# Performance work log

Hardware: AMD Instinct MI355X
Metric: run time of the kernel (lower is better)

The kernel has to match this reference:

```python
import jax, jax.numpy as jnp
import numpy as np

NPOINT, RADIUS, NSAMPLE, EPS = 1024, 0.2, 32, 1e-5


def furthest_point_sample(xyz, npoint):
    # xyz: [B,N,3] -> idx [B,npoint] int32. Sequential FPS starting at index 0
    # (matches pointnet2 CUDA kernel initialization).
    B, N, _ = xyz.shape
    dist0 = jnp.full((B, N), 1e10, xyz.dtype)
    far0 = jnp.zeros((B,), jnp.int32)
    idx0 = jnp.zeros((B, npoint), jnp.int32)  # idx[:,0] = 0

    def body(i, state):
        idx, dist, far = state
        centroid = jnp.take_along_axis(xyz, far[:, None, None], axis=1)  # [B,1,3]
        d = jnp.sum((xyz - centroid) ** 2, axis=-1)                       # [B,N]
        dist = jnp.minimum(dist, d)
        far = jnp.argmax(dist, axis=1).astype(jnp.int32)
        return idx.at[:, i].set(far), dist, far

    idx, _, _ = jax.lax.fori_loop(1, npoint, body, (idx0, dist0, far0))
    return idx


def ball_query(radius, nsample, xyz, new_xyz):
    # xyz [B,N,3], new_xyz [B,S,3] -> idx [B,S,nsample] int32.
    # First nsample points (in original order) within radius; slots with no
    # neighbor are filled with the first found index (standard pointnet2 semantics).
    B, N, _ = xyz.shape
    S = new_xyz.shape[1]
    d2 = (jnp.sum(new_xyz ** 2, -1)[:, :, None]
          + jnp.sum(xyz ** 2, -1)[:, None, :]
          - 2.0 * jnp.einsum('bsc,bnc->bsn', new_xyz, xyz))  # [B,S,N]
    grp = jnp.broadcast_to(jnp.arange(N, dtype=jnp.int32), (B, S, N))
    grp = jnp.where(d2 > radius * radius, N, grp)
    grp = jnp.sort(grp, axis=-1)[:, :, :nsample]
    first = grp[:, :, :1]
    return jnp.where(grp == N, first, grp)


def _gather(pts, idx):
    # pts [B,N,C], idx [B,...] -> [B,...,C]
    return jax.vmap(lambda p, i: p[i])(pts, idx)


def setup_inputs() -> dict:
    key = jax.random.key(0)
    ks = jax.random.split(key, 32)
    B, N, D = 16, 4096, 64
    mlp = [64, 64, 128]
    inp = {
        'xyz': jax.random.uniform(ks[0], (B, N, 3), jnp.float32),
        'points': jax.random.normal(ks[1], (B, N, D), jnp.float32),
    }
    cprev = 3 + D
    for i, cout in enumerate(mlp):
        kk = ks[2 + 4 * i: 6 + 4 * i]
        inp[f'W{i}'] = jax.random.normal(kk[0], (cout, cprev), jnp.float32) / np.float32(np.sqrt(cprev))
        inp[f'b{i}'] = jax.random.normal(kk[1], (cout,), jnp.float32) * 0.01
        inp[f'g{i}'] = 1.0 + 0.1 * jax.random.normal(kk[2], (cout,), jnp.float32)
        inp[f'beta{i}'] = 0.1 * jax.random.normal(kk[3], (cout,), jnp.float32)
        inp[f'm{i}'] = jnp.zeros((cout,), jnp.float32)
        inp[f'v{i}'] = jnp.ones((cout,), jnp.float32)
        cprev = cout
    return inp


def reference(xyz, points, W0, b0, g0, beta0, m0, v0,
              W1, b1, g1, beta1, m1, v1,
              W2, b2, g2, beta2, m2, v2):
    fps_idx = furthest_point_sample(xyz, NPOINT)
    new_xyz = _gather(xyz, fps_idx)                       # [B,S,3]
    idx = ball_query(RADIUS, NSAMPLE, xyz, new_xyz)       # [B,S,K]
    grouped_xyz = _gather(xyz, idx)                       # [B,S,K,3]
    grouped_norm = grouped_xyz - new_xyz[:, :, None, :]
    grouped_pts = _gather(points, idx)                    # [B,S,K,D]
    h = jnp.concatenate([grouped_norm, grouped_pts], axis=-1)  # [B,S,K,3+D]
    layers = [(W0, b0, g0, beta0, m0, v0), (W1, b1, g1, beta1, m1, v1), (W2, b2, g2, beta2, m2, v2)]
    for W, b, g, be, m, v in layers:
        h = jnp.einsum('oc,bskc->bsko', W, h) + b          # 1x1 conv
        h = (h - m) * (g * jax.lax.rsqrt(v + EPS)) + be    # eval-mode BN
        h = jax.nn.relu(h)
    new_points = jnp.max(h, axis=2)                        # max over nsample -> [B,S,Cout]
    return new_xyz, new_points
```

## Files before the change

kernel.cpp:

```cpp
#include <hip/hip_runtime.h>

#define N_PTS  4096
#define N_CENT 1024
#define K_S    32
#define EPSV   1e-5f

typedef __attribute__((ext_vector_type(8))) short short8;
typedef __attribute__((ext_vector_type(4))) float floatx4;
typedef __attribute__((ext_vector_type(2))) float float2v;

__device__ inline unsigned short bf1(float x) {
  unsigned u = __float_as_uint(x);
  u += 0x7fffu + ((u >> 16) & 1u);
  return (unsigned short)(u >> 16);
}
__device__ inline unsigned pkbf(float a, float b) {
  return (unsigned)bf1(a) | ((unsigned)bf1(b) << 16);
}

__global__ void prep_kernel(const float* __restrict__ W0, const float* __restrict__ b0,
                            const float* __restrict__ g0, const float* __restrict__ be0,
                            const float* __restrict__ m0, const float* __restrict__ v0,
                            const float* __restrict__ W1, const float* __restrict__ b1,
                            const float* __restrict__ g1, const float* __restrict__ be1,
                            const float* __restrict__ m1, const float* __restrict__ v1,
                            const float* __restrict__ W2, const float* __restrict__ b2,
                            const float* __restrict__ g2, const float* __restrict__ be2,
                            const float* __restrict__ m2, const float* __restrict__ v2,
                            unsigned char* __restrict__ wsb) {
  const int stride = gridDim.x * blockDim.x;
  const int tid = blockIdx.x * blockDim.x + threadIdx.x;
  unsigned short* WB0 = (unsigned short*)wsb;
  unsigned short* WB1 = (unsigned short*)(wsb + 12288);
  unsigned short* WB2 = (unsigned short*)(wsb + 20480);
  float* Bf0 = (float*)(wsb + 36864);
  float* Bf1 = (float*)(wsb + 37120);
  float* Bf2 = (float*)(wsb + 37376);
  for (int i = tid; i < 64 * 96; i += stride) {
    int o = i / 96, k = i - o * 96;
    float s = g0[o] * rsqrtf(v0[o] + EPSV);
    float val = 0.0f;
    if (k < 64) val = W0[o * 67 + 3 + k] * s;
    else if (k < 67) val = W0[o * 67 + (k - 64)] * s;
    WB0[i] = bf1(val);
  }
  for (int i = tid; i < 64; i += stride) {
    float s = g0[i] * rsqrtf(v0[i] + EPSV);
    Bf0[i] = (b0[i] - m0[i]) * s + be0[i];
  }
  for (int i = tid; i < 64 * 64; i += stride) {
    int o = i >> 6;
    float s = g1[o] * rsqrtf(v1[o] + EPSV);
    WB1[i] = bf1(W1[i] * s);
  }
  for (int i = tid; i < 64; i += stride) {
    float s = g1[i] * rsqrtf(v1[i] + EPSV);
    Bf1[i] = (b1[i] - m1[i]) * s + be1[i];
  }
  for (int i = tid; i < 128 * 64; i += stride) {
    int o = i >> 6;
    float s = g2[o] * rsqrtf(v2[o] + EPSV);
    WB2[i] = bf1(W2[i] * s);
  }
  for (int i = tid; i < 128; i += stride) {
    float s = g2[i] * rsqrtf(v2[i] + EPSV);
    Bf2[i] = (b2[i] - m2[i]) * s + be2[i];
  }
}

#define DPP_STEP(CTRL)                                                               \
  {                                                                                  \
    unsigned lo2 = (unsigned)__builtin_amdgcn_update_dpp(                            \
        0, (int)(unsigned)key, (CTRL), 0xf, 0xf, false);                             \
    unsigned hi2 = (unsigned)__builtin_amdgcn_update_dpp(                            \
        0, (int)(unsigned)(key >> 32), (CTRL), 0xf, 0xf, false);                     \
    unsigned long long nk = ((unsigned long long)hi2 << 32) | lo2;                   \
    if (nk > key) key = nk;                                                          \
  }

__launch_bounds__(256)
__global__ void fps_kernel(const float* __restrict__ xyz, float* __restrict__ new_xyz) {
#pragma clang fp contract(off)
  const int b = blockIdx.x;
  const int tid = threadIdx.x;
  const int lane = tid & 63, wv = tid >> 6;
  const float* X = xyz + (size_t)b * N_PTS * 3;
  __shared__ float lx[N_PTS], ly[N_PTS], lz[N_PTS];
  __shared__ float cent[N_CENT * 3];
  __shared__ unsigned long long rkey[2][4];
  float2v px[8], py[8], pz[8], dist[8];
#pragma unroll
  for (int j = 0; j < 16; ++j) {
    int p = j * 256 + tid;
    float x = X[p * 3 + 0], y = X[p * 3 + 1], z = X[p * 3 + 2];
    lx[p] = x; ly[p] = y; lz[p] = z;
    int t = j >> 1;
    if ((j & 1) == 0) { px[t].x = x; py[t].x = y; pz[t].x = z; dist[t].x = 1e10f; }
    else              { px[t].y = x; py[t].y = y; pz[t].y = z; dist[t].y = 1e10f; }
  }
  if (tid == 0) { cent[0] = X[0]; cent[1] = X[1]; cent[2] = X[2]; }
  __syncthreads();
  int far = 0;
  for (int i = 1; i < N_CENT; ++i) {
    float cx = lx[far], cy = ly[far], cz = lz[far];
    float2v cx2 = {cx, cx}, cy2 = {cy, cy}, cz2 = {cz, cz};
    float best = -1.0f;
    int bi = 0;
#pragma unroll
    for (int t = 0; t < 8; ++t) {
      float2v dx = px[t] - cx2, dy = py[t] - cy2, dz = pz[t] - cz2;
      float2v d2 = dx * dx + dy * dy + dz * dz;
      float d0 = fminf(dist[t].x, d2.x); dist[t].x = d0;
      if (d0 > best) { best = d0; bi = (2 * t) * 256 + tid; }
      float d1 = fminf(dist[t].y, d2.y); dist[t].y = d1;
      if (d1 > best) { best = d1; bi = (2 * t + 1) * 256 + tid; }
    }
    unsigned long long key =
        ((unsigned long long)__float_as_uint(best) << 32) | (unsigned)(~bi);
    DPP_STEP(0x111);
    DPP_STEP(0x112);
    DPP_STEP(0x114);
    DPP_STEP(0x118);
    DPP_STEP(0x142);
    DPP_STEP(0x143);
    const int par = i & 1;
    if (lane == 63) rkey[par][wv] = key;
    __syncthreads();
    unsigned long long k0 = rkey[par][0], k1 = rkey[par][1];
    unsigned long long k2 = rkey[par][2], k3 = rkey[par][3];
    if (k1 > k0) k0 = k1;
    if (k3 > k2) k2 = k3;
    if (k2 > k0) k0 = k2;
    far = (int)~(unsigned)k0;
    if (tid == 0) {
      cent[i * 3 + 0] = lx[far];
      cent[i * 3 + 1] = ly[far];
      cent[i * 3 + 2] = lz[far];
    }
  }
  __syncthreads();
  const size_t ob = (size_t)b * N_CENT * 3;
  for (int t = tid; t < N_CENT * 3; t += 256) new_xyz[ob + t] = cent[t];
}

__launch_bounds__(256)
__global__ void query_kernel(const float* __restrict__ xyz,
                             const float* __restrict__ new_xyz,
                             int* __restrict__ nid_g) {
#pragma clang fp contract(off)
  const int blk = blockIdx.x;
  const int b = blk >> 7;
  const int s0 = (blk & 127) << 3;
  const int tid = threadIdx.x;
  const int wv = tid >> 6, lane = tid & 63;
  const float* Xb = xyz + (size_t)b * N_PTS * 3;
  const float r2 = (float)(0.2 * 0.2);
  const int sA = s0 + wv * 2, sB = sA + 1;
  float cxA = new_xyz[((size_t)b * N_CENT + sA) * 3 + 0];
  float cyA = new_xyz[((size_t)b * N_CENT + sA) * 3 + 1];
  float czA = new_xyz[((size_t)b * N_CENT + sA) * 3 + 2];
  float cxB = new_xyz[((size_t)b * N_CENT + sB) * 3 + 0];
  float cyB = new_xyz[((size_t)b * N_CENT + sB) * 3 + 1];
  float czB = new_xyz[((size_t)b * N_CENT + sB) * 3 + 2];
  float scA = cxA * cxA + cyA * cyA + czA * czA;
  float scB = cxB * cxB + cyB * cyB + czB * czB;
  int* outA = nid_g + ((size_t)b * N_CENT + sA) * K_S;
  int* outB = nid_g + ((size_t)b * N_CENT + sB) * K_S;
  int cntA = 0, cntB = 0, firstA = 0, firstB = 0;
  for (int base = 0; base < N_PTS && (cntA < K_S || cntB < K_S); base += 64) {
    int p = base + lane;
    float x = Xb[p * 3 + 0], y = Xb[p * 3 + 1], z = Xb[p * 3 + 2];
    float sp = x * x + y * y + z * z;
    float dtA = __builtin_fmaf(czA, z, __builtin_fmaf(cyA, y, cxA * x));
    float dtB = __builtin_fmaf(czB, z, __builtin_fmaf(cyB, y, cxB * x));
    float d2A = (scA + sp) - 2.0f * dtA;
    float d2B = (scB + sp) - 2.0f * dtB;
    bool inA = !(d2A > r2);
    bool inB = !(d2B > r2);
    unsigned long long mA = __ballot(inA);
    unsigned long long mB = __ballot(inB);
    if (cntA == 0 && mA != 0ull) firstA = base + __builtin_ctzll(mA);
    if (cntB == 0 && mB != 0ull) firstB = base + __builtin_ctzll(mB);
    unsigned long long below = (1ull << lane) - 1ull;
    int posA = cntA + __popcll(mA & below);
    int posB = cntB + __popcll(mB & below);
    if (inA && posA < K_S) outA[posA] = p;
    if (inB && posB < K_S) outB[posB] = p;
    cntA += __popcll(mA);
    cntB += __popcll(mB);
  }
  if (cntA < K_S)
    for (int j = cntA + lane; j < K_S; j += 64) outA[j] = firstA;
  if (cntB < K_S)
    for (int j = cntB + lane; j < K_S; j += 64) outB[j] = firstB;
}

__launch_bounds__(256)
__global__ void mlp_kernel(const float* __restrict__ xyz,
                           const float* __restrict__ points,
                           const float* __restrict__ new_xyz,
                           const unsigned char* __restrict__ wsb,
                           const int* __restrict__ nid_g,
                           float* __restrict__ out_pts) {
  __shared__ __align__(16) unsigned short h[256 * 104];
  const int blk = blockIdx.x;
  const int b = blk >> 7;
  const int s0 = (blk & 127) << 3;
  const int tid = threadIdx.x;
  const float* Xb = xyz + (size_t)b * N_PTS * 3;

  {
    const int s = s0 + (tid >> 5);
    const int id = nid_g[((size_t)b * N_CENT + s0) * K_S + tid];
    float cx = new_xyz[((size_t)b * N_CENT + s) * 3 + 0];
    float cy = new_xyz[((size_t)b * N_CENT + s) * 3 + 1];
    float cz = new_xyz[((size_t)b * N_CENT + s) * 3 + 2];
    float gx = Xb[id * 3 + 0] - cx;
    float gy = Xb[id * 3 + 1] - cy;
    float gz = Xb[id * 3 + 2] - cz;
    unsigned short* hrow = &h[tid * 104];
    const float4* P = (const float4*)(points + ((size_t)b * N_PTS + id) * 64);
#pragma unroll
    for (int c8 = 0; c8 < 8; ++c8) {
      float4 u = P[2 * c8], v = P[2 * c8 + 1];
      uint4 w4;
      w4.x = pkbf(u.x, u.y); w4.y = pkbf(u.z, u.w);
      w4.z = pkbf(v.x, v.y); w4.w = pkbf(v.z, v.w);
      *(uint4*)(hrow + c8 * 8) = w4;
    }
    uint4 t4;
    t4.x = pkbf(gx, gy); t4.y = pkbf(gz, 0.0f); t4.z = 0u; t4.w = 0u;
    *(uint4*)(hrow + 64) = t4;
    uint4 z4; z4.x = z4.y = z4.z = z4.w = 0u;
    *(uint4*)(hrow + 72) = z4;
    *(uint4*)(hrow + 80) = z4;
    *(uint4*)(hrow + 88) = z4;
  }
  __syncthreads();

  const int lane = tid & 63, w = tid >> 6;
  const int col = lane & 15, kq = lane >> 4;
  const unsigned short* WB0 = (const unsigned short*)wsb;
  const unsigned short* WB1 = (const unsigned short*)(wsb + 12288);
  const unsigned short* WB2 = (const unsigned short*)(wsb + 20480);
  const float* Bf0 = (const float*)(wsb + 36864);
  const float* Bf1 = (const float*)(wsb + 37120);
  const float* Bf2 = (const float*)(wsb + 37376);

  {
    const int o = w * 16 + col;
    float bias = Bf0[o];
    floatx4 acc[16];
#pragma unroll
    for (int mt = 0; mt < 16; ++mt) acc[mt] = floatx4{bias, bias, bias, bias};
#pragma unroll
    for (int c = 0; c < 3; ++c) {
      short8 bf = *(const short8*)(WB0 + o * 96 + kq * 8 + 32 * c);
#pragma unroll
      for (int mt = 0; mt < 16; ++mt) {
        short8 af = *(const short8*)(&h[(mt * 16 + col) * 104 + kq * 8 + 32 * c]);
        acc[mt] = __builtin_amdgcn_mfma_f32_16x16x32_bf16(af, bf, acc[mt], 0, 0, 0);
      }
    }
    __syncthreads();
#pragma unroll
    for (int mt = 0; mt < 16; ++mt)
#pragma unroll
      for (int r = 0; r < 4; ++r)
        h[(mt * 16 + kq * 4 + r) * 104 + o] = bf1(fmaxf(acc[mt][r], 0.0f));
    __syncthreads();
  }

  {
    const int o = w * 16 + col;
    float bias = Bf1[o];
    floatx4 acc[16];
#pragma unroll
    for (int mt = 0; mt < 16; ++mt) acc[mt] = floatx4{bias, bias, bias, bias};
#pragma unroll
    for (int c = 0; c < 2; ++c) {
      short8 bf = *(const short8*)(WB1 + o * 64 + kq * 8 + 32 * c);
#pragma unroll
      for (int mt = 0; mt < 16; ++mt) {
        short8 af = *(const short8*)(&h[(mt * 16 + col) * 104 + kq * 8 + 32 * c]);
        acc[mt] = __builtin_amdgcn_mfma_f32_16x16x32_bf16(af, bf, acc[mt], 0, 0, 0);
      }
    }
    __syncthreads();
#pragma unroll
    for (int mt = 0; mt < 16; ++mt)
#pragma unroll
      for (int r = 0; r < 4; ++r)
        h[(mt * 16 + kq * 4 + r) * 104 + o] = bf1(fmaxf(acc[mt][r], 0.0f));
    __syncthreads();
  }

  {
    const int oA = w * 32 + col;
    const int oB = oA + 16;
    float biasA = Bf2[oA], biasB = Bf2[oB];
    floatx4 accA[16], accB[16];
#pragma unroll
    for (int mt = 0; mt < 16; ++mt) {
      accA[mt] = floatx4{biasA, biasA, biasA, biasA};
      accB[mt] = floatx4{biasB, biasB, biasB, biasB};
    }
#pragma unroll
    for (int c = 0; c < 2; ++c) {
      short8 bfA = *(const short8*)(WB2 + oA * 64 + kq * 8 + 32 * c);
      short8 bfB = *(const short8*)(WB2 + oB * 64 + kq * 8 + 32 * c);
#pragma unroll
      for (int mt = 0; mt < 16; ++mt) {
        short8 af = *(const short8*)(&h[(mt * 16 + col) * 104 + kq * 8 + 32 * c]);
        accA[mt] = __builtin_amdgcn_mfma_f32_16x16x32_bf16(af, bfA, accA[mt], 0, 0, 0);
        accB[mt] = __builtin_amdgcn_mfma_f32_16x16x32_bf16(af, bfB, accB[mt], 0, 0, 0);
      }
    }
#pragma unroll
    for (int mtp = 0; mtp < 8; ++mtp) {
      float vA = fmaxf(fmaxf(fmaxf(accA[2 * mtp][0], accA[2 * mtp + 1][0]),
                             fmaxf(accA[2 * mtp][1], accA[2 * mtp + 1][1])),
                       fmaxf(fmaxf(accA[2 * mtp][2], accA[2 * mtp + 1][2]),
                             fmaxf(accA[2 * mtp][3], accA[2 * mtp + 1][3])));
      float vB = fmaxf(fmaxf(fmaxf(accB[2 * mtp][0], accB[2 * mtp + 1][0]),
                             fmaxf(accB[2 * mtp][1], accB[2 * mtp + 1][1])),
                       fmaxf(fmaxf(accB[2 * mtp][2], accB[2 * mtp + 1][2]),
                             fmaxf(accB[2 * mtp][3], accB[2 * mtp + 1][3])));
      vA = fmaxf(vA, __shfl_xor(vA, 16)); vA = fmaxf(vA, __shfl_xor(vA, 32));
      vB = fmaxf(vB, __shfl_xor(vB, 16)); vB = fmaxf(vB, __shfl_xor(vB, 32));
      vA = fmaxf(vA, 0.0f); vB = fmaxf(vB, 0.0f);
      if (lane < 16) {
        float* op = out_pts + ((size_t)(b * N_CENT + s0 + mtp)) * 128;
        op[oA] = vA;
        op[oB] = vB;
      }
    }
  }
}

extern "C" void kernel_launch(void* const* d_in, const int* in_sizes, int n_in,
                              void* d_out, int out_size, void* d_ws, size_t ws_size,
                              hipStream_t stream) {
  const float* xyz = (const float*)d_in[0];
  const float* points = (const float*)d_in[1];
  float* out = (float*)d_out;
  float* new_xyz = out;
  float* out_pts = out + 16 * 1024 * 3;
  unsigned char* wsb = (unsigned char*)d_ws;
  int* nid_g = (int*)(wsb + 65536);

  prep_kernel<<<64, 256, 0, stream>>>(
      (const float*)d_in[2], (const float*)d_in[3], (const float*)d_in[4],
      (const float*)d_in[5], (const float*)d_in[6], (const float*)d_in[7],
      (const float*)d_in[8], (const float*)d_in[9], (const float*)d_in[10],
      (const float*)d_in[11], (const float*)d_in[12], (const float*)d_in[13],
      (const float*)d_in[14], (const float*)d_in[15], (const float*)d_in[16],
      (const float*)d_in[17], (const float*)d_in[18], (const float*)d_in[19], wsb);
  fps_kernel<<<16, 256, 0, stream>>>(xyz, new_xyz);
  query_kernel<<<2048, 256, 0, stream>>>(xyz, new_xyz, nid_g);
  mlp_kernel<<<2048, 256, 0, stream>>>(xyz, points, new_xyz, wsb, nid_g, out_pts);
}
```

Measured before the change: 798.3 us.

## Fuse FPS, ball query and MLP into one persistent kernel with progress flags

```diff
diff --git a/kernel.cpp b/kernel.cpp
--- a/kernel.cpp
+++ b/kernel.cpp
@@ -36,6 +36,8 @@
   float* Bf0 = (float*)(wsb + 36864);
   float* Bf1 = (float*)(wsb + 37120);
   float* Bf2 = (float*)(wsb + 37376);
+  int* prog = (int*)(wsb + 40960);
+  if (tid < 16) prog[tid] = 0;
   for (int i = tid; i < 64 * 96; i += stride) {
     int o = i / 96, k = i - o * 96;
     float s = g0[o] * rsqrtf(v0[o] + EPSV);
@@ -79,262 +81,283 @@
   }
 
 __launch_bounds__(256)
-__global__ void fps_kernel(const float* __restrict__ xyz, float* __restrict__ new_xyz) {
-#pragma clang fp contract(off)
-  const int b = blockIdx.x;
+__global__ void fused_kernel(const float* __restrict__ xyz,
+                             const float* __restrict__ points,
+                             const unsigned char* __restrict__ wsb,
+                             float* __restrict__ new_xyz,
+                             float* __restrict__ out_pts,
+                             int* __restrict__ progress) {
+  __shared__ __align__(16) union SM {
+    struct {
+      float lx[N_PTS], ly[N_PTS], lz[N_PTS];
+      float cent[N_CENT * 3];
+      unsigned long long rkey[2][4];
+    } f;
+    struct {
+      unsigned short h[256 * 104];
+      int nidx[256];
+    } c;
+  } sm;
   const int tid = threadIdx.x;
   const int lane = tid & 63, wv = tid >> 6;
-  const float* X = xyz + (size_t)b * N_PTS * 3;
-  __shared__ float lx[N_PTS], ly[N_PTS], lz[N_PTS];
-  __shared__ float cent[N_CENT * 3];
-  __shared__ unsigned long long rkey[2][4];
-  float2v px[8], py[8], pz[8], dist[8];
-#pragma unroll
-  for (int j = 0; j < 16; ++j) {
-    int p = j * 256 + tid;
-    float x = X[p * 3 + 0], y = X[p * 3 + 1], z = X[p * 3 + 2];
-    lx[p] = x; ly[p] = y; lz[p] = z;
-    int t = j >> 1;
-    if ((j & 1) == 0) { px[t].x = x; py[t].x = y; pz[t].x = z; dist[t].x = 1e10f; }
-    else              { px[t].y = x; py[t].y = y; pz[t].y = z; dist[t].y = 1e10f; }
-  }
-  if (tid == 0) { cent[0] = X[0]; cent[1] = X[1]; cent[2] = X[2]; }
-  __syncthreads();
-  int far = 0;
-  for (int i = 1; i < N_CENT; ++i) {
-    float cx = lx[far], cy = ly[far], cz = lz[far];
-    float2v cx2 = {cx, cx}, cy2 = {cy, cy}, cz2 = {cz, cz};
-    float best = -1.0f;
-    int bi = 0;
-#pragma unroll
-    for (int t = 0; t < 8; ++t) {
-      float2v dx = px[t] - cx2, dy = py[t] - cy2, dz = pz[t] - cz2;
-      float2v d2 = dx * dx + dy * dy + dz * dz;
-      float d0 = fminf(dist[t].x, d2.x); dist[t].x = d0;
-      if (d0 > best) { best = d0; bi = (2 * t) * 256 + tid; }
-      float d1 = fminf(dist[t].y, d2.y); dist[t].y = d1;
-      if (d1 > best) { best = d1; bi = (2 * t + 1) * 256 + tid; }
-    }
-    unsigned long long key =
-        ((unsigned long long)__float_as_uint(best) << 32) | (unsigned)(~bi);
-    DPP_STEP(0x111);
-    DPP_STEP(0x112);
-    DPP_STEP(0x114);
-    DPP_STEP(0x118);
-    DPP_STEP(0x142);
-    DPP_STEP(0x143);
-    const int par = i & 1;
-    if (lane == 63) rkey[par][wv] = key;
-    __syncthreads();
-    unsigned long long k0 = rkey[par][0], k1 = rkey[par][1];
-    unsigned long long k2 = rkey[par][2], k3 = rkey[par][3];
-    if (k1 > k0) k0 = k1;
-    if (k3 > k2) k2 = k3;
-    if (k2 > k0) k0 = k2;
-    far = (int)~(unsigned)k0;
+
+  if (blockIdx.x < 16) {
+#pragma clang fp contract(off)
+    const int b = blockIdx.x;
+    const float* X = xyz + (size_t)b * N_PTS * 3;
+    const size_t ob = (size_t)b * N_CENT * 3;
+    float2v px[8], py[8], pz[8], dist[8];
+#pragma unroll
+    for (int j = 0; j < 16; ++j) {
+      int p = j * 256 + tid;
+      float x = X[p * 3 + 0], y = X[p * 3 + 1], z = X[p * 3 + 2];
+      sm.f.lx[p] = x; sm.f.ly[p] = y; sm.f.lz[p] = z;
+      int t = j >> 1;
+      if ((j & 1) == 0) { px[t].x = x; py[t].x = y; pz[t].x = z; dist[t].x = 1e10f; }
+      else              { px[t].y = x; py[t].y = y; pz[t].y = z; dist[t].y = 1e10f; }
+    }
+    if (tid == 0) { sm.f.cent[0] = X[0]; sm.f.cent[1] = X[1]; sm.f.cent[2] = X[2]; }
+    __syncthreads();
+    int far = 0;
+    for (int i = 1; i < N_CENT; ++i) {
+      if ((i & 63) == 0) {
+        __syncthreads();
+        const int k = (i >> 6) - 1;
+        if (tid < 192) new_xyz[ob + k * 192 + tid] = sm.f.cent[k * 192 + tid];
+        __syncthreads();
+        if (tid == 0) {
+          __threadfence();
+          __hip_atomic_store(progress + b, i, __ATOMIC_RELEASE,
+                             __HIP_MEMORY_SCOPE_AGENT);
+        }
+      }
+      float cx = sm.f.lx[far], cy = sm.f.ly[far], cz = sm.f.lz[far];
+      float2v cx2 = {cx, cx}, cy2 = {cy, cy}, cz2 = {cz, cz};
+      float best = -1.0f;
+      int bi = 0;
+#pragma unroll
+      for (int t = 0; t < 8; ++t) {
+        float2v dx = px[t] - cx2, dy = py[t] - cy2, dz = pz[t] - cz2;
+        float2v d2 = dx * dx + dy * dy + dz * dz;
+        float d0 = fminf(dist[t].x, d2.x); dist[t].x = d0;
+        if (d0 > best) { best = d0; bi = (2 * t) * 256 + tid; }
+        float d1 = fminf(dist[t].y, d2.y); dist[t].y = d1;
+        if (d1 > best) { best = d1; bi = (2 * t + 1) * 256 + tid; }
+      }
+      unsigned long long key =
+          ((unsigned long long)__float_as_uint(best) << 32) | (unsigned)(~bi);
+      DPP_STEP(0x111);
+      DPP_STEP(0x112);
+      DPP_STEP(0x114);
+      DPP_STEP(0x118);
+      DPP_STEP(0x142);
+      DPP_STEP(0x143);
+      const int par = i & 1;
+      if (lane == 63) sm.f.rkey[par][wv] = key;
+      __syncthreads();
+      unsigned long long k0 = sm.f.rkey[par][0], k1 = sm.f.rkey[par][1];
+      unsigned long long k2 = sm.f.rkey[par][2], k3 = sm.f.rkey[par][3];
+      if (k1 > k0) k0 = k1;
+      if (k3 > k2) k2 = k3;
+      if (k2 > k0) k0 = k2;
+      far = (int)~(unsigned)k0;
+      if (tid == 0) {
+        sm.f.cent[i * 3 + 0] = sm.f.lx[far];
+        sm.f.cent[i * 3 + 1] = sm.f.ly[far];
+        sm.f.cent[i * 3 + 2] = sm.f.lz[far];
+      }
+    }
+    __syncthreads();
+    if (tid < 192) new_xyz[ob + 15 * 192 + tid] = sm.f.cent[15 * 192 + tid];
+    __syncthreads();
     if (tid == 0) {
-      cent[i * 3 + 0] = lx[far];
-      cent[i * 3 + 1] = ly[far];
-      cent[i * 3 + 2] = lz[far];
-    }
-  }
-  __syncthreads();
-  const size_t ob = (size_t)b * N_CENT * 3;
-  for (int t = tid; t < N_CENT * 3; t += 256) new_xyz[ob + t] = cent[t];
-}
-
-__launch_bounds__(256)
-__global__ void query_kernel(const float* __restrict__ xyz,
-                             const float* __restrict__ new_xyz,
-                             int* __restrict__ nid_g) {
-#pragma clang fp contract(off)
-  const int blk = blockIdx.x;
-  const int b = blk >> 7;
-  const int s0 = (blk & 127) << 3;
-  const int tid = threadIdx.x;
-  const int wv = tid >> 6, lane = tid & 63;
-  const float* Xb = xyz + (size_t)b * N_PTS * 3;
-  const float r2 = (float)(0.2 * 0.2);
-  const int sA = s0 + wv * 2, sB = sA + 1;
-  float cxA = new_xyz[((size_t)b * N_CENT + sA) * 3 + 0];
-  float cyA = new_xyz[((size_t)b * N_CENT + sA) * 3 + 1];
-  float czA = new_xyz[((size_t)b * N_CENT + sA) * 3 + 2];
-  float cxB = new_xyz[((size_t)b * N_CENT + sB) * 3 + 0];
-  float cyB = new_xyz[((size_t)b * N_CENT + sB) * 3 + 1];
-  float czB = new_xyz[((size_t)b * N_CENT + sB) * 3 + 2];
-  float scA = cxA * cxA + cyA * cyA + czA * czA;
-  float scB = cxB * cxB + cyB * cyB + czB * czB;
-  int* outA = nid_g + ((size_t)b * N_CENT + sA) * K_S;
-  int* outB = nid_g + ((size_t)b * N_CENT + sB) * K_S;
-  int cntA = 0, cntB = 0, firstA = 0, firstB = 0;
-  for (int base = 0; base < N_PTS && (cntA < K_S || cntB < K_S); base += 64) {
-    int p = base + lane;
-    float x = Xb[p * 3 + 0], y = Xb[p * 3 + 1], z = Xb[p * 3 + 2];
-    float sp = x * x + y * y + z * z;
-    float dtA = __builtin_fmaf(czA, z, __builtin_fmaf(cyA, y, cxA * x));
-    float dtB = __builtin_fmaf(czB, z, __builtin_fmaf(cyB, y, cxB * x));
-    float d2A = (scA + sp) - 2.0f * dtA;
-    float d2B = (scB + sp) - 2.0f * dtB;
-    bool inA = !(d2A > r2);
-    bool inB = !(d2B > r2);
-    unsigned long long mA = __ballot(inA);
-    unsigned long long mB = __ballot(inB);
-    if (cntA == 0 && mA != 0ull) firstA = base + __builtin_ctzll(mA);
-    if (cntB == 0 && mB != 0ull) firstB = base + __builtin_ctzll(mB);
-    unsigned long long below = (1ull << lane) - 1ull;
-    int posA = cntA + __popcll(mA & below);
-    int posB = cntB + __popcll(mB & below);
-    if (inA && posA < K_S) outA[posA] = p;
-    if (inB && posB < K_S) outB[posB] = p;
-    cntA += __popcll(mA);
-    cntB += __popcll(mB);
-  }
-  if (cntA < K_S)
-    for (int j = cntA + lane; j < K_S; j += 64) outA[j] = firstA;
-  if (cntB < K_S)
-    for (int j = cntB + lane; j < K_S; j += 64) outB[j] = firstB;
-}
-
-__launch_bounds__(256)
-__global__ void mlp_kernel(const float* __restrict__ xyz,
-                           const float* __restrict__ points,
-                           const float* __restrict__ new_xyz,
-                           const unsigned char* __restrict__ wsb,
-                           const int* __restrict__ nid_g,
-                           float* __restrict__ out_pts) {
-  __shared__ __align__(16) unsigned short h[256 * 104];
-  const int blk = blockIdx.x;
-  const int b = blk >> 7;
-  const int s0 = (blk & 127) << 3;
-  const int tid = threadIdx.x;
-  const float* Xb = xyz + (size_t)b * N_PTS * 3;
-
-  {
-    const int s = s0 + (tid >> 5);
-    const int id = nid_g[((size_t)b * N_CENT + s0) * K_S + tid];
-    float cx = new_xyz[((size_t)b * N_CENT + s) * 3 + 0];
-    float cy = new_xyz[((size_t)b * N_CENT + s) * 3 + 1];
-    float cz = new_xyz[((size_t)b * N_CENT + s) * 3 + 2];
-    float gx = Xb[id * 3 + 0] - cx;
-    float gy = Xb[id * 3 + 1] - cy;
-    float gz = Xb[id * 3 + 2] - cz;
-    unsigned short* hrow = &h[tid * 104];
-    const float4* P = (const float4*)(points + ((size_t)b * N_PTS + id) * 64);
-#pragma unroll
-    for (int c8 = 0; c8 < 8; ++c8) {
-      float4 u = P[2 * c8], v = P[2 * c8 + 1];
-      uint4 w4;
-      w4.x = pkbf(u.x, u.y); w4.y = pkbf(u.z, u.w);
-      w4.z = pkbf(v.x, v.y); w4.w = pkbf(v.z, v.w);
-      *(uint4*)(hrow + c8 * 8) = w4;
-    }
-    uint4 t4;
-    t4.x = pkbf(gx, gy); t4.y = pkbf(gz, 0.0f); t4.z = 0u; t4.w = 0u;
-    *(uint4*)(hrow + 64) = t4;
-    uint4 z4; z4.x = z4.y = z4.z = z4.w = 0u;
-    *(uint4*)(hrow + 72) = z4;
-    *(uint4*)(hrow + 80) = z4;
-    *(uint4*)(hrow + 88) = z4;
-  }
-  __syncthreads();
-
-  const int lane = tid & 63, w = tid >> 6;
-  const int col = lane & 15, kq = lane >> 4;
+      __threadfence();
+      __hip_atomic_store(progress + b, 1024, __ATOMIC_RELEASE,
+                         __HIP_MEMORY_SCOPE_AGENT);
+    }
+    return;
+  }
+
   const unsigned short* WB0 = (const unsigned short*)wsb;
   const unsigned short* WB1 = (const unsigned short*)(wsb + 12288);
   const unsigned short* WB2 = (const unsigned short*)(wsb + 20480);
   const float* Bf0 = (const float*)(wsb + 36864);
   const float* Bf1 = (const float*)(wsb + 37120);
   const float* Bf2 = (const float*)(wsb + 37376);
-
-  {
-    const int o = w * 16 + col;
-    float bias = Bf0[o];
-    floatx4 acc[16];
-#pragma unroll
-    for (int mt = 0; mt < 16; ++mt) acc[mt] = floatx4{bias, bias, bias, bias};
-#pragma unroll
-    for (int c = 0; c < 3; ++c) {
-      short8 bf = *(const short8*)(WB0 + o * 96 + kq * 8 + 32 * c);
+  const int cid = blockIdx.x - 16;
+
+  for (int g = cid; g < 2048; g += 240) {
+    const int k = g >> 7, rem = g & 127, b = rem >> 3, u = rem & 7;
+    const int s0 = k * 64 + u * 8;
+    if (tid == 0) {
+      while (__hip_atomic_load(progress + b, __ATOMIC_ACQUIRE,
+                               __HIP_MEMORY_SCOPE_AGENT) < s0 + 8)
+        __builtin_amdgcn_s_sleep(32);
+    }
+    __syncthreads();
+
+    const float* Xb = xyz + (size_t)b * N_PTS * 3;
+    {
+#pragma clang fp contract(off)
+      const float r2 = (float)(0.2 * 0.2);
+      const int sA = s0 + wv * 2, sB = sA + 1;
+      float cxA = new_xyz[((size_t)b * N_CENT + sA) * 3 + 0];
+      float cyA = new_xyz[((size_t)b * N_CENT + sA) * 3 + 1];
+      float czA = new_xyz[((size_t)b * N_CENT + sA) * 3 + 2];
+      float cxB = new_xyz[((size_t)b * N_CENT + sB) * 3 + 0];
+      float cyB = new_xyz[((size_t)b * N_CENT + sB) * 3 + 1];
+      float czB = new_xyz[((size_t)b * N_CENT + sB) * 3 + 2];
+      float scA = cxA * cxA + cyA * cyA + czA * czA;
+      float scB = cxB * cxB + cyB * cyB + czB * czB;
+      int cntA = 0, cntB = 0, firstA = 0, firstB = 0;
+      for (int base = 0; base < N_PTS && (cntA < K_S || cntB < K_S); base += 64) {
+        int p = base + lane;
+        float x = Xb[p * 3 + 0], y = Xb[p * 3 + 1], z = Xb[p * 3 + 2];
+        float sp = x * x + y * y + z * z;
+        float dtA = __builtin_fmaf(czA, z, __builtin_fmaf(cyA, y, cxA * x));
+        float dtB = __builtin_fmaf(czB, z, __builtin_fmaf(cyB, y, cxB * x));
+        float d2A = (scA + sp) - 2.0f * dtA;
+        float d2B = (scB + sp) - 2.0f * dtB;
+        bool inA = !(d2A > r2);
+        bool inB = !(d2B > r2);
+        unsigned long long mA = __ballot(inA);
+        unsigned long long mB = __ballot(inB);
+        if (cntA == 0 && mA != 0ull) firstA = base + __builtin_ctzll(mA);
+        if (cntB == 0 && mB != 0ull) firstB = base + __builtin_ctzll(mB);
+        unsigned long long below = (1ull << lane) - 1ull;
+        int posA = cntA + __popcll(mA & below);
+        int posB = cntB + __popcll(mB & below);
+        if (inA && posA < K_S) sm.c.nidx[(wv * 2 + 0) * K_S + posA] = p;
+        if (inB && posB < K_S) sm.c.nidx[(wv * 2 + 1) * K_S + posB] = p;
+        cntA += __popcll(mA);
+        cntB += __popcll(mB);
+      }
+      if (cntA < K_S)
+        for (int j = cntA + lane; j < K_S; j += 64) sm.c.nidx[(wv * 2 + 0) * K_S + j] = firstA;
+      if (cntB < K_S)
+        for (int j = cntB + lane; j < K_S; j += 64) sm.c.nidx[(wv * 2 + 1) * K_S + j] = firstB;
+    }
+    __syncthreads();
+
+    {
+      const int s = s0 + (tid >> 5);
+      const int id = sm.c.nidx[tid];
+      float cx = new_xyz[((size_t)b * N_CENT + s) * 3 + 0];
+      float cy = new_xyz[((size_t)b * N_CENT + s) * 3 + 1];
+      float cz = new_xyz[((size_t)b * N_CENT + s) * 3 + 2];
+      float gx = Xb[id * 3 + 0] - cx;
+      float gy = Xb[id * 3 + 1] - cy;
+      float gz = Xb[id * 3 + 2] - cz;
+      unsigned short* hrow = &sm.c.h[tid * 104];
+      const float4* P = (const float4*)(points + ((size_t)b * N_PTS + id) * 64);
+#pragma unroll
+      for (int c8 = 0; c8 < 8; ++c8) {
+        float4 uu = P[2 * c8], vv = P[2 * c8 + 1];
+        uint4 w4;
+        w4.x = pkbf(uu.x, uu.y); w4.y = pkbf(uu.z, uu.w);
+        w4.z = pkbf(vv.x, vv.y); w4.w = pkbf(vv.z, vv.w);
+        *(uint4*)(hrow + c8 * 8) = w4;
+      }
+      uint4 t4;
+      t4.x = pkbf(gx, gy); t4.y = pkbf(gz, 0.0f); t4.z = 0u; t4.w = 0u;
+      *(uint4*)(hrow + 64) = t4;
+      uint4 z4; z4.x = z4.y = z4.z = z4.w = 0u;
+      *(uint4*)(hrow + 72) = z4;
+      *(uint4*)(hrow + 80) = z4;
+      *(uint4*)(hrow + 88) = z4;
+    }
+    __syncthreads();
+
+    const int col = lane & 15, kq = lane >> 4;
+    const int w = wv;
+    {
+      const int o = w * 16 + col;
+      float bias = Bf0[o];
+      floatx4 acc[16];
+#pragma unroll
+      for (int mt = 0; mt < 16; ++mt) acc[mt] = floatx4{bias, bias, bias, bias};
+#pragma unroll
+      for (int c = 0; c < 3; ++c) {
+        short8 bf = *(const short8*)(WB0 + o * 96 + kq * 8 + 32 * c);
+#pragma unroll
+        for (int mt = 0; mt < 16; ++mt) {
+          short8 af = *(const short8*)(&sm.c.h[(mt * 16 + col) * 104 + kq * 8 + 32 * c]);
+          acc[mt] = __builtin_amdgcn_mfma_f32_16x16x32_bf16(af, bf, acc[mt], 0, 0, 0);
+        }
+      }
+      __syncthreads();
+#pragma unroll
+      for (int mt = 0; mt < 16; ++mt)
+#pragma unroll
+        for (int r = 0; r < 4; ++r)
+          sm.c.h[(mt * 16 + kq * 4 + r) * 104 + o] = bf1(fmaxf(acc[mt][r], 0.0f));
+      __syncthreads();
+    }
+    {
+      const int o = w * 16 + col;
+      float bias = Bf1[o];
+      floatx4 acc[16];
+#pragma unroll
+      for (int mt = 0; mt < 16; ++mt) acc[mt] = floatx4{bias, bias, bias, bias};
+#pragma unroll
+      for (int c = 0; c < 2; ++c) {
+        short8 bf = *(const short8*)(WB1 + o * 64 + kq * 8 + 32 * c);
+#pragma unroll
+        for (int mt = 0; mt < 16; ++mt) {
+          short8 af = *(const short8*)(&sm.c.h[(mt * 16 + col) * 104 + kq * 8 + 32 * c]);
+          acc[mt] = __builtin_amdgcn_mfma_f32_16x16x32_bf16(af, bf, acc[mt], 0, 0, 0);
+        }
+      }
+      __syncthreads();
+#pragma unroll
+      for (int mt = 0; mt < 16; ++mt)
+#pragma unroll
+        for (int r = 0; r < 4; ++r)
+          sm.c.h[(mt * 16 + kq * 4 + r) * 104 + o] = bf1(fmaxf(acc[mt][r], 0.0f));
+      __syncthreads();
+    }
+    {
+      const int oA = w * 32 + col;
+      const int oB = oA + 16;
+      float biasA = Bf2[oA], biasB = Bf2[oB];
+      floatx4 accA[16], accB[16];
 #pragma unroll
       for (int mt = 0; mt < 16; ++mt) {
-        short8 af = *(const short8*)(&h[(mt * 16 + col) * 104 + kq * 8 + 32 * c]);
-        acc[mt] = __builtin_amdgcn_mfma_f32_16x16x32_bf16(af, bf, acc[mt], 0, 0, 0);
-      }
-    }
-    __syncthreads();
-#pragma unroll
-    for (int mt = 0; mt < 16; ++mt)
-#pragma unroll
-      for (int r = 0; r < 4; ++r)
-        h[(mt * 16 + kq * 4 + r) * 104 + o] = bf1(fmaxf(acc[mt][r], 0.0f));
-    __syncthreads();
-  }
-
-  {
-    const int o = w * 16 + col;
-    float bias = Bf1[o];
-    floatx4 acc[16];
-#pragma unroll
-    for (int mt = 0; mt < 16; ++mt) acc[mt] = floatx4{bias, bias, bias, bias};
-#pragma unroll
-    for (int c = 0; c < 2; ++c) {
-      short8 bf = *(const short8*)(WB1 + o * 64 + kq * 8 + 32 * c);
-#pragma unroll
-      for (int mt = 0; mt < 16; ++mt) {
-        short8 af = *(const short8*)(&h[(mt * 16 + col) * 104 + kq * 8 + 32 * c]);
-        acc[mt] = __builtin_amdgcn_mfma_f32_16x16x32_bf16(af, bf, acc[mt], 0, 0, 0);
-      }
-    }
-    __syncthreads();
-#pragma unroll
-    for (int mt = 0; mt < 16; ++mt)
-#pragma unroll
-      for (int r = 0; r < 4; ++r)
-        h[(mt * 16 + kq * 4 + r) * 104 + o] = bf1(fmaxf(acc[mt][r], 0.0f));
-    __syncthreads();
-  }
-
-  {
-    const int oA = w * 32 + col;
-    const int oB = oA + 16;
-    float biasA = Bf2[oA], biasB = Bf2[oB];
-    floatx4 accA[16], accB[16];
-#pragma unroll
-    for (int mt = 0; mt < 16; ++mt) {
-      accA[mt] = floatx4{biasA, biasA, biasA, biasA};
-      accB[mt] = floatx4{biasB, biasB, biasB, biasB};
-    }
-#pragma unroll
-    for (int c = 0; c < 2; ++c) {
-      short8 bfA = *(const short8*)(WB2 + oA * 64 + kq * 8 + 32 * c);
-      short8 bfB = *(const short8*)(WB2 + oB * 64 + kq * 8 + 32 * c);
-#pragma unroll
-      for (int mt = 0; mt < 16; ++mt) {
-        short8 af = *(const short8*)(&h[(mt * 16 + col) * 104 + kq * 8 + 32 * c]);
-        accA[mt] = __builtin_amdgcn_mfma_f32_16x16x32_bf16(af, bfA, accA[mt], 0, 0, 0);
-        accB[mt] = __builtin_amdgcn_mfma_f32_16x16x32_bf16(af, bfB, accB[mt], 0, 0, 0);
-      }
-    }
-#pragma unroll
-    for (int mtp = 0; mtp < 8; ++mtp) {
-      float vA = fmaxf(fmaxf(fmaxf(accA[2 * mtp][0], accA[2 * mtp + 1][0]),
-                             fmaxf(accA[2 * mtp][1], accA[2 * mtp + 1][1])),
-                       fmaxf(fmaxf(accA[2 * mtp][2], accA[2 * mtp + 1][2]),
-                             fmaxf(accA[2 * mtp][3], accA[2 * mtp + 1][3])));
-      float vB = fmaxf(fmaxf(fmaxf(accB[2 * mtp][0], accB[2 * mtp + 1][0]),
-                             fmaxf(accB[2 * mtp][1], accB[2 * mtp + 1][1])),
-                       fmaxf(fmaxf(accB[2 * mtp][2], accB[2 * mtp + 1][2]),
-                             fmaxf(accB[2 * mtp][3], accB[2 * mtp + 1][3])));
-      vA = fmaxf(vA, __shfl_xor(vA, 16)); vA = fmaxf(vA, __shfl_xor(vA, 32));
-      vB = fmaxf(vB, __shfl_xor(vB, 16)); vB = fmaxf(vB, __shfl_xor(vB, 32));
-      vA = fmaxf(vA, 0.0f); vB = fmaxf(vB, 0.0f);
-      if (lane < 16) {
-        float* op = out_pts + ((size_t)(b * N_CENT + s0 + mtp)) * 128;
-        op[oA] = vA;
-        op[oB] = vB;
-      }
-    }
+        accA[mt] = floatx4{biasA, biasA, biasA, biasA};
+        accB[mt] = floatx4{biasB, biasB, biasB, biasB};
+      }
+#pragma unroll
+      for (int c = 0; c < 2; ++c) {
+        short8 bfA = *(const short8*)(WB2 + oA * 64 + kq * 8 + 32 * c);
+        short8 bfB = *(const short8*)(WB2 + oB * 64 + kq * 8 + 32 * c);
+#pragma unroll
+        for (int mt = 0; mt < 16; ++mt) {
+          short8 af = *(const short8*)(&sm.c.h[(mt * 16 + col) * 104 + kq * 8 + 32 * c]);
+          accA[mt] = __builtin_amdgcn_mfma_f32_16x16x32_bf16(af, bfA, accA[mt], 0, 0, 0);
+          accB[mt] = __builtin_amdgcn_mfma_f32_16x16x32_bf16(af, bfB, accB[mt], 0, 0, 0);
+        }
+      }
+#pragma unroll
+      for (int mtp = 0; mtp < 8; ++mtp) {
+        float vA = fmaxf(fmaxf(fmaxf(accA[2 * mtp][0], accA[2 * mtp + 1][0]),
+                               fmaxf(accA[2 * mtp][1], accA[2 * mtp + 1][1])),
+                         fmaxf(fmaxf(accA[2 * mtp][2], accA[2 * mtp + 1][2]),
+                               fmaxf(accA[2 * mtp][3], accA[2 * mtp + 1][3])));
+        float vB = fmaxf(fmaxf(fmaxf(accB[2 * mtp][0], accB[2 * mtp + 1][0]),
+                               fmaxf(accB[2 * mtp][1], accB[2 * mtp + 1][1])),
+                         fmaxf(fmaxf(accB[2 * mtp][2], accB[2 * mtp + 1][2]),
+                               fmaxf(accB[2 * mtp][3], accB[2 * mtp + 1][3])));
+        vA = fmaxf(vA, __shfl_xor(vA, 16)); vA = fmaxf(vA, __shfl_xor(vA, 32));
+        vB = fmaxf(vB, __shfl_xor(vB, 16)); vB = fmaxf(vB, __shfl_xor(vB, 32));
+        vA = fmaxf(vA, 0.0f); vB = fmaxf(vB, 0.0f);
+        if (lane < 16) {
+          float* op = out_pts + ((size_t)(b * N_CENT + s0 + mtp)) * 128;
+          op[oA] = vA;
+          op[oB] = vB;
+        }
+      }
+    }
+    __syncthreads();
   }
 }
 
@@ -347,7 +370,7 @@
   float* new_xyz = out;
   float* out_pts = out + 16 * 1024 * 3;
   unsigned char* wsb = (unsigned char*)d_ws;
-  int* nid_g = (int*)(wsb + 65536);
+  int* progress = (int*)(wsb + 40960);
 
   prep_kernel<<<64, 256, 0, stream>>>(
       (const float*)d_in[2], (const float*)d_in[3], (const float*)d_in[4],
@@ -356,7 +379,7 @@
       (const float*)d_in[11], (const float*)d_in[12], (const float*)d_in[13],
       (const float*)d_in[14], (const float*)d_in[15], (const float*)d_in[16],
       (const float*)d_in[17], (const float*)d_in[18], (const float*)d_in[19], wsb);
-  fps_kernel<<<16, 256, 0, stream>>>(xyz, new_xyz);
-  query_kernel<<<2048, 256, 0, stream>>>(xyz, new_xyz, nid_g);
-  mlp_kernel<<<2048, 256, 0, stream>>>(xyz, points, new_xyz, wsb, nid_g, out_pts);
-}
+
+  fused_kernel<<<256, 256, 0, stream>>>(xyz, points, wsb, new_xyz, out_pts,
+                                        progress);
+}
```

New measurement: 830.6 us. 4.1% more time.
